# Kernel optimization log

Measured on AMD Instinct MI355X. Metric: run time of the kernel, lower is better.

The kernel has to match this reference:

```python
import jax, jax.numpy as jnp
import numpy as np
import math

DIM = 512
HID = 2048
BS, SLEN = 4, 4096


def _bayes_linear(x, mu, log_sigma, eps):
    # torchbnn BayesLinear: W = mu + exp(log_sigma) * eps; y = x @ W^T
    W = mu + jnp.exp(log_sigma) * eps
    return jnp.einsum('...i,oi->...o', x, W)


def setup_inputs() -> dict:
    key = jax.random.key(0)
    ks = jax.random.split(key, 20)
    d = {}
    d['x'] = jax.random.normal(ks[0], (BS, SLEN, DIM), dtype=jnp.float32)
    # causal additive mask, broadcast over batch
    causal = jnp.triu(jnp.full((SLEN, SLEN), -1e9, dtype=jnp.float32), k=1)
    d['mask'] = causal[None, :, :]
    shapes = {'wk': (DIM, DIM), 'wv': (DIM, DIM), 'wo': (DIM, DIM), 'w1': (HID, DIM), 'w2': (DIM, HID)}
    i = 1
    for name, shp in shapes.items():
        fan_in = shp[1]
        d[name + '_mu'] = jax.random.normal(ks[i], shp, dtype=jnp.float32) / np.sqrt(fan_in); i += 1
        d[name + '_ls'] = (-3.0 + 0.1 * jax.random.normal(ks[i], shp, dtype=jnp.float32)); i += 1
        d[name + '_eps'] = jax.random.normal(ks[i], shp, dtype=jnp.float32); i += 1
    return d


def reference(x, mask, wk_mu, wk_ls, wk_eps, wv_mu, wv_ls, wv_eps, wo_mu, wo_ls, wo_eps,
              w1_mu, w1_ls, w1_eps, w2_mu, w2_ls, w2_eps):
    dim = x.shape[-1]
    # attention: W_q is identity
    xq = x
    xk = _bayes_linear(x, wk_mu, wk_ls, wk_eps)
    xv = _bayes_linear(x, wv_mu, wv_ls, wv_eps)
    scores = jnp.einsum('bqd,bkd->bqk', xq, xk) / math.sqrt(dim) + mask
    attn = jax.nn.softmax(scores, axis=-1)
    h = jnp.einsum('bqk,bkd->bqd', attn, xv)
    h_attn = _bayes_linear(h, wo_mu, wo_ls, wo_eps)
    h_res = x + h_attn
    # FFN with ReLU
    ff = _bayes_linear(h_res, w1_mu, w1_ls, w1_eps)
    ff = jax.nn.relu(ff)
    ff = _bayes_linear(ff, w2_mu, w2_ls, w2_eps)
    return h_res + ff
```

## Files before the change

### kernel.cpp

```cpp
#include <hip/hip_runtime.h>
#include <hip/hip_bf16.h>

typedef __hip_bfloat16 bf16;
typedef __attribute__((ext_vector_type(8))) short short8;
typedef __attribute__((ext_vector_type(4))) float f32x4;

#define MFMA16(a,b,c) __builtin_amdgcn_mfma_f32_16x16x32_bf16(a,b,c,0,0,0)

__device__ __forceinline__ void gl_lds16(const void* g, void* l) {
  __builtin_amdgcn_global_load_lds(
      (const __attribute__((address_space(1))) void*)g,
      (__attribute__((address_space(3))) void*)l, 16, 0, 0);
}

__global__ __launch_bounds__(256) void prep_kernel(
    const float* __restrict__ x,
    const float* __restrict__ m0, const float* __restrict__ l0, const float* __restrict__ e0,
    const float* __restrict__ m1, const float* __restrict__ l1, const float* __restrict__ e1,
    const float* __restrict__ m2, const float* __restrict__ l2, const float* __restrict__ e2,
    const float* __restrict__ m3, const float* __restrict__ l3, const float* __restrict__ e3,
    const float* __restrict__ m4, const float* __restrict__ l4, const float* __restrict__ e4,
    bf16* __restrict__ xb, bf16* __restrict__ wts)
{
  long e = ((long)blockIdx.x * 256 + threadIdx.x) * 4;
  if (e < 8388608L) {
    float4 v = *(const float4*)(x + e);
    union { bf16 b[4]; short4 s; } u;
    u.b[0] = __float2bfloat16(v.x); u.b[1] = __float2bfloat16(v.y);
    u.b[2] = __float2bfloat16(v.z); u.b[3] = __float2bfloat16(v.w);
    *(short4*)(xb + e) = u.s;
  } else {
    long we = e - 8388608L;
    const float *mu, *ls, *ep; long off = we;
    if (we < 262144L)        { mu = m0; ls = l0; ep = e0; }
    else if (we < 524288L)   { mu = m1; ls = l1; ep = e1; off = we - 262144L; }
    else if (we < 786432L)   { mu = m2; ls = l2; ep = e2; off = we - 524288L; }
    else if (we < 1835008L)  { mu = m3; ls = l3; ep = e3; off = we - 786432L; }
    else                     { mu = m4; ls = l4; ep = e4; off = we - 1835008L; }
    float4 a = *(const float4*)(mu + off);
    float4 b = *(const float4*)(ls + off);
    float4 c = *(const float4*)(ep + off);
    union { bf16 w[4]; short4 s; } u;
    u.w[0] = __float2bfloat16(a.x + __expf(b.x) * c.x);
    u.w[1] = __float2bfloat16(a.y + __expf(b.y) * c.y);
    u.w[2] = __float2bfloat16(a.z + __expf(b.z) * c.z);
    u.w[3] = __float2bfloat16(a.w + __expf(b.w) * c.w);
    *(short4*)(wts + we) = u.s;
  }
}

template<int MODE>
__global__ __launch_bounds__(256, 2) void gemm_nt(
    const bf16* __restrict__ A, const bf16* __restrict__ B,
    const float* __restrict__ resid, float* __restrict__ outf,
    bf16* __restrict__ outb, int M, int N, int K)
{
  __shared__ bf16 As[128 * 32];
  __shared__ bf16 Bs[128 * 32];
  const int t = threadIdx.x, w = t >> 6, lane = t & 63;
  const int quad = lane >> 4, c16 = lane & 15;
  const int bm = blockIdx.x << 7, bn = blockIdx.y << 7;
  const int wr = (w >> 1) << 6, wc = (w & 1) << 6;

  f32x4 acc[4][4] = {};

  const int srow = t >> 2;
  const int scol = (t & 3) * 8;
  const bf16* Ab = A + (long)bm * K;
  const bf16* Bb = B + (long)bn * K;

  for (int k0 = 0; k0 < K; k0 += 32) {
    gl_lds16(Ab + (long)srow * K + k0 + scol,        (char*)As + (w << 10));
    gl_lds16(Ab + (long)(64 + srow) * K + k0 + scol, (char*)As + 4096 + (w << 10));
    gl_lds16(Bb + (long)srow * K + k0 + scol,        (char*)Bs + (w << 10));
    gl_lds16(Bb + (long)(64 + srow) * K + k0 + scol, (char*)Bs + 4096 + (w << 10));
    __syncthreads();
    short8 a[4], b[4];
    #pragma unroll
    for (int i = 0; i < 4; i++)
      a[i] = *(const short8*)(As + (wr + i * 16 + c16) * 32 + quad * 8);
    #pragma unroll
    for (int j = 0; j < 4; j++)
      b[j] = *(const short8*)(Bs + (wc + j * 16 + c16) * 32 + quad * 8);
    #pragma unroll
    for (int i = 0; i < 4; i++)
      #pragma unroll
      for (int j = 0; j < 4; j++)
        acc[i][j] = MFMA16(a[i], b[j], acc[i][j]);
    __syncthreads();
  }

  #pragma unroll
  for (int i = 0; i < 4; i++) {
    const int row = bm + wr + i * 16 + quad * 4;
    #pragma unroll
    for (int j = 0; j < 4; j++) {
      const int col = bn + wc + j * 16 + c16;
      #pragma unroll
      for (int r = 0; r < 4; r++) {
        float v = acc[i][j][r];
        if (MODE == 4) {
          int n = (row + r) & 31;
          long idx = (long)(row + r) * 512 + ((((col >> 3) ^ (n & 7)) << 3) | (col & 7));
          outb[idx] = __float2bfloat16(v);
        } else if (MODE == 5) {
          int g = row + r;
          int kvl = g & 31;
          long idx = (((long)(g >> 5)) << 14) + (long)col * 32 +
                     (((kvl >> 3) ^ ((col >> 1) & 3)) << 3) + (kvl & 7);
          outb[idx] = __float2bfloat16(v);
        } else {
          long idx = (long)(row + r) * N + col;
          if (MODE == 0) {
            outb[idx] = __float2bfloat16(v);
          } else if (MODE == 1) {
            float vv = v + resid[idx];
            outf[idx] = vv;
            outb[idx] = __float2bfloat16(vv);
          } else if (MODE == 2) {
            outb[idx] = __float2bfloat16(v > 0.f ? v : 0.f);
          } else {
            outf[idx] = v + resid[idx];
          }
        }
      }
    }
  }
}

__global__ __launch_bounds__(256, 2) void attn3_kernel(
    const bf16* __restrict__ xq, const bf16* __restrict__ xkS,
    const bf16* __restrict__ xvS, bf16* __restrict__ Opart,
    float* __restrict__ lsum)
{
  __shared__ bf16 Ks[32 * 512];
  __shared__ bf16 Vs[512 * 32];
  __shared__ bf16 Pb[4 * 512];

  const int t = threadIdx.x, w = t >> 6, lane = t & 63;
  const int quad = lane >> 4, c16 = lane & 15;
  const int n = blockIdx.x;
  const int B = n & 3, h = (n >> 2) & 1, i = n >> 3;
  const long boff = (long)B * (4096L * 512);
  const float scale = 0.04419417382415922f;
  const float FM = 30.0f;

  union { short8 s; short u[8]; } ones;
  #pragma unroll
  for (int k = 0; k < 8; k++) ones.u[k] = (short)0x3F80;

  for (int seg = 0; seg < 2; seg++) {
    const int qt = seg ? (63 - i) : i;
    const int nt = qt + 1;
    const int t0 = h * nt;
    const int qb = qt << 6;

    short8 qf[16];
    {
      const bf16* qrow = xq + boff + (long)(qb + w * 16 + c16) * 512 + quad * 8;
      #pragma unroll
      for (int f = 0; f < 16; f++) qf[f] = *(const short8*)(qrow + f * 32);
    }

    f32x4 o[32];
    #pragma unroll
    for (int jj = 0; jj < 32; jj++) o[jj] = (f32x4){0.f, 0.f, 0.f, 0.f};
    f32x4 lacc = (f32x4){0.f, 0.f, 0.f, 0.f};

    for (int tt = 0; tt < nt; ++tt) {
      const int tile = t0 + tt;
      const int kv0 = tile << 5;
      {
        const long tb = ((long)(B * 128 + tile)) << 14;
        const bf16* ks = xkS + tb + (w << 9) + (lane << 3);
        const bf16* vs = xvS + tb + (w << 9) + (lane << 3);
        char* kd = (char*)Ks + (w << 10);
        char* vd = (char*)Vs + (w << 10);
        #pragma unroll
        for (int r2 = 0; r2 < 8; r2++) {
          gl_lds16(ks + (r2 << 11), kd + (r2 << 12));
          gl_lds16(vs + (r2 << 11), vd + (r2 << 12));
        }
      }
      __syncthreads();

      f32x4 s0 = (f32x4){0.f, 0.f, 0.f, 0.f};
      f32x4 s1 = s0;
      const int n0 = c16, n1 = 16 + c16;
      const int sw0 = (c16 & 7) << 3;
      #pragma unroll
      for (int f = 0; f < 16; f++) {
        int cb = (f * 4 + quad) << 3;
        short8 b0 = *(const short8*)(Ks + n0 * 512 + (cb ^ sw0));
        short8 b1 = *(const short8*)(Ks + n1 * 512 + (cb ^ sw0));
        s0 = MFMA16(qf[f], b0, s0);
        s1 = MFMA16(qf[f], b1, s1);
      }

      bf16* Pw = Pb + (w << 9);
      {
        const int qr0 = qb + w * 16 + quad * 4;
        const bool need_mask = (kv0 + 32 > qb);
        #pragma unroll
        for (int r = 0; r < 4; r++) {
          float p0 = __expf(fmaf(s0[r], scale, -FM));
          float p1 = __expf(fmaf(s1[r], scale, -FM));
          if (need_mask) {
            if (kv0 + n0 > qr0 + r) p0 = 0.f;
            if (kv0 + n1 > qr0 + r) p1 = 0.f;
          }
          int pr = quad * 4 + r;
          int swp = (pr >> 1) & 3;
          Pw[pr * 32 + (((n0 >> 3) ^ swp) << 3) + (n0 & 7)] = __float2bfloat16(p0);
          Pw[pr * 32 + (((n1 >> 3) ^ swp) << 3) + (n1 & 7)] = __float2bfloat16(p1);
        }
      }
      short8 pa = *(const short8*)(Pw + c16 * 32 + ((quad ^ ((c16 >> 1) & 3)) << 3));
      lacc = MFMA16(pa, ones.s, lacc);
      #pragma unroll
      for (int jj = 0; jj < 32; jj++) {
        int d = jj * 16 + c16;
        short8 vb = *(const short8*)(Vs + d * 32 + ((quad ^ ((d >> 1) & 3)) << 3));
        o[jj] = MFMA16(pa, vb, o[jj]);
      }
      __syncthreads();
    }

    const int pidx = (B * 64 + qt) * 2 + h;
    {
      bf16* ob = Opart + ((long)pidx << 15) + (long)(w * 16 + quad * 4) * 512 + c16;
      #pragma unroll
      for (int r = 0; r < 4; r++) {
        #pragma unroll
        for (int jj = 0; jj < 32; jj++)
          ob[(long)r * 512 + jj * 16] = __float2bfloat16(o[jj][r]);
      }
      if (c16 == 0) {
        #pragma unroll
        for (int r = 0; r < 4; r++)
          lsum[pidx * 64 + w * 16 + quad * 4 + r] = lacc[r];
      }
    }
  }
}

__global__ __launch_bounds__(256) void combine_kernel(
    const bf16* __restrict__ Opart, const float* __restrict__ lsum,
    bf16* __restrict__ hb)
{
  const int t = threadIdx.x;
  const int r = blockIdx.x * 4 + (t >> 6);
  const int B = r >> 12, rl = r & 4095, qt = rl >> 6, rr = rl & 63;
  const int pA = (B * 64 + qt) * 2, pB = pA + 1;
  float inv = 1.0f / (lsum[pA * 64 + rr] + lsum[pB * 64 + rr]);
  const int d0 = (t & 63) * 8;
  union { short8 s; bf16 b[8]; } ua, ub, uo;
  ua.s = *(const short8*)(Opart + (((long)pA << 6) + rr) * 512 + d0);
  ub.s = *(const short8*)(Opart + (((long)pB << 6) + rr) * 512 + d0);
  #pragma unroll
  for (int k = 0; k < 8; k++)
    uo.b[k] = __float2bfloat16((__bfloat162float(ua.b[k]) + __bfloat162float(ub.b[k])) * inv);
  *(short8*)(hb + (long)r * 512 + d0) = uo.s;
}

extern "C" void kernel_launch(void* const* d_in, const int* in_sizes, int n_in,
                              void* d_out, int out_size, void* d_ws, size_t ws_size,
                              hipStream_t stream) {
  (void)in_sizes; (void)n_in; (void)out_size; (void)ws_size;
  const float* x = (const float*)d_in[0];
  const float* wk_mu = (const float*)d_in[2],  *wk_ls = (const float*)d_in[3],  *wk_eps = (const float*)d_in[4];
  const float* wv_mu = (const float*)d_in[5],  *wv_ls = (const float*)d_in[6],  *wv_eps = (const float*)d_in[7];
  const float* wo_mu = (const float*)d_in[8],  *wo_ls = (const float*)d_in[9],  *wo_eps = (const float*)d_in[10];
  const float* w1_mu = (const float*)d_in[11], *w1_ls = (const float*)d_in[12], *w1_eps = (const float*)d_in[13];
  const float* w2_mu = (const float*)d_in[14], *w2_ls = (const float*)d_in[15], *w2_eps = (const float*)d_in[16];

  const long MB = 1048576L;
  char* ws = (char*)d_ws;
  bf16*   xb    = (bf16*)(ws + 0);
  bf16*   xkS   = (bf16*)(ws + 16 * MB);
  bf16*   xvS   = (bf16*)(ws + 32 * MB);
  bf16*   Opart = (bf16*)(ws + 48 * MB);
  float*  lsb   = (float*)(ws + 80 * MB);
  bf16*   wts   = (bf16*)(ws + 113 * MB);
  bf16*   hb    = (bf16*)(ws + 32 * MB);
  bf16*   hrb   = (bf16*)(ws + 64 * MB);
  float*  hrf   = (float*)(ws + 81 * MB);
  bf16*   ffb   = (bf16*)(ws + 0);

  bf16* wkb = wts;
  bf16* wvb = wts + 262144;
  bf16* wob = wts + 524288;
  bf16* w1b = wts + 786432;
  bf16* w2b = wts + 1835008;

  prep_kernel<<<11008, 256, 0, stream>>>(x,
      wk_mu, wk_ls, wk_eps, wv_mu, wv_ls, wv_eps, wo_mu, wo_ls, wo_eps,
      w1_mu, w1_ls, w1_eps, w2_mu, w2_ls, w2_eps, xb, wts);

  gemm_nt<4><<<dim3(128, 4),  256, 0, stream>>>(xb,  wkb, nullptr, nullptr, xkS, 16384, 512, 512);
  gemm_nt<5><<<dim3(128, 4),  256, 0, stream>>>(xb,  wvb, nullptr, nullptr, xvS, 16384, 512, 512);

  attn3_kernel<<<256, 256, 0, stream>>>(xb, xkS, xvS, Opart, lsb);
  combine_kernel<<<4096, 256, 0, stream>>>(Opart, lsb, hb);

  gemm_nt<1><<<dim3(128, 4),  256, 0, stream>>>(hb,  wob, x,   hrf, hrb, 16384, 512, 512);
  gemm_nt<2><<<dim3(128, 16), 256, 0, stream>>>(hrb, w1b, nullptr, nullptr, ffb, 16384, 2048, 512);
  gemm_nt<3><<<dim3(128, 4),  256, 0, stream>>>(ffb, w2b, hrf, (float*)d_out, nullptr, 16384, 512, 2048);
}
```

Measured before the change: 538.8 us.

## Split attention KV range four ways with strided tiles and four-way combine

The attention kernel now splits each query tile's KV range across four blocks (interleaved tiles with stride 4) instead of two contiguous halves, launching 512 blocks instead of 256. The combine kernel sums four partial outputs and four partial row sums. The workspace layout is rearranged to fit the doubled partial buffer. The aim is better CU occupancy and load balance across the 256 CUs. In exchange, the partial outputs written and read back double, and Q fragments are reloaded by more blocks.

```diff
diff --git a/kernel.cpp b/kernel.cpp
--- a/kernel.cpp
+++ b/kernel.cpp
@@ -128,7 +128,7 @@
   }
 }
 
-__global__ __launch_bounds__(256, 2) void attn3_kernel(
+__global__ __launch_bounds__(256, 2) void attn4_kernel(
     const bf16* __restrict__ xq, const bf16* __restrict__ xkS,
     const bf16* __restrict__ xvS, bf16* __restrict__ Opart,
     float* __restrict__ lsum)
@@ -140,7 +140,7 @@
   const int t = threadIdx.x, w = t >> 6, lane = t & 63;
   const int quad = lane >> 4, c16 = lane & 15;
   const int n = blockIdx.x;
-  const int B = n & 3, h = (n >> 2) & 1, i = n >> 3;
+  const int B = n & 3, par = (n >> 2) & 3, i = n >> 4;
   const long boff = (long)B * (4096L * 512);
   const float scale = 0.04419417382415922f;
   const float FM = 30.0f;
@@ -151,8 +151,7 @@
 
   for (int seg = 0; seg < 2; seg++) {
     const int qt = seg ? (63 - i) : i;
-    const int nt = qt + 1;
-    const int t0 = h * nt;
+    const int T = 2 * (qt + 1);
     const int qb = qt << 6;
 
     short8 qf[16];
@@ -167,8 +166,7 @@
     for (int jj = 0; jj < 32; jj++) o[jj] = (f32x4){0.f, 0.f, 0.f, 0.f};
     f32x4 lacc = (f32x4){0.f, 0.f, 0.f, 0.f};
 
-    for (int tt = 0; tt < nt; ++tt) {
-      const int tile = t0 + tt;
+    for (int tile = par; tile < T; tile += 4) {
       const int kv0 = tile << 5;
       {
         const long tb = ((long)(B * 128 + tile)) << 14;
@@ -226,7 +224,7 @@
       __syncthreads();
     }
 
-    const int pidx = (B * 64 + qt) * 2 + h;
+    const int pidx = (B * 64 + qt) * 4 + par;
     {
       bf16* ob = Opart + ((long)pidx << 15) + (long)(w * 16 + quad * 4) * 512 + c16;
       #pragma unroll
@@ -251,15 +249,22 @@
   const int t = threadIdx.x;
   const int r = blockIdx.x * 4 + (t >> 6);
   const int B = r >> 12, rl = r & 4095, qt = rl >> 6, rr = rl & 63;
-  const int pA = (B * 64 + qt) * 2, pB = pA + 1;
-  float inv = 1.0f / (lsum[pA * 64 + rr] + lsum[pB * 64 + rr]);
+  const int p0 = (B * 64 + qt) * 4;
+  float lt = lsum[p0 * 64 + rr] + lsum[(p0 + 1) * 64 + rr] +
+             lsum[(p0 + 2) * 64 + rr] + lsum[(p0 + 3) * 64 + rr];
+  float inv = 1.0f / lt;
   const int d0 = (t & 63) * 8;
-  union { short8 s; bf16 b[8]; } ua, ub, uo;
-  ua.s = *(const short8*)(Opart + (((long)pA << 6) + rr) * 512 + d0);
-  ub.s = *(const short8*)(Opart + (((long)pB << 6) + rr) * 512 + d0);
+  union { short8 s; bf16 b[8]; } u0, u1, u2, u3, uo;
+  u0.s = *(const short8*)(Opart + (((long)(p0 + 0) << 6) + rr) * 512 + d0);
+  u1.s = *(const short8*)(Opart + (((long)(p0 + 1) << 6) + rr) * 512 + d0);
+  u2.s = *(const short8*)(Opart + (((long)(p0 + 2) << 6) + rr) * 512 + d0);
+  u3.s = *(const short8*)(Opart + (((long)(p0 + 3) << 6) + rr) * 512 + d0);
   #pragma unroll
-  for (int k = 0; k < 8; k++)
-    uo.b[k] = __float2bfloat16((__bfloat162float(ua.b[k]) + __bfloat162float(ub.b[k])) * inv);
+  for (int k = 0; k < 8; k++) {
+    float s = __bfloat162float(u0.b[k]) + __bfloat162float(u1.b[k]) +
+              __bfloat162float(u2.b[k]) + __bfloat162float(u3.b[k]);
+    uo.b[k] = __float2bfloat16(s * inv);
+  }
   *(short8*)(hb + (long)r * 512 + d0) = uo.s;
 }
 
@@ -280,11 +285,11 @@
   bf16*   xkS   = (bf16*)(ws + 16 * MB);
   bf16*   xvS   = (bf16*)(ws + 32 * MB);
   bf16*   Opart = (bf16*)(ws + 48 * MB);
-  float*  lsb   = (float*)(ws + 80 * MB);
+  float*  lsb   = (float*)(ws + 112 * MB);
   bf16*   wts   = (bf16*)(ws + 113 * MB);
   bf16*   hb    = (bf16*)(ws + 32 * MB);
-  bf16*   hrb   = (bf16*)(ws + 64 * MB);
-  float*  hrf   = (float*)(ws + 81 * MB);
+  float*  hrf   = (float*)(ws + 64 * MB);
+  bf16*   hrb   = (bf16*)(ws + 96 * MB);
   bf16*   ffb   = (bf16*)(ws + 0);
 
   bf16* wkb = wts;
@@ -300,7 +305,7 @@
   gemm_nt<4><<<dim3(128, 4),  256, 0, stream>>>(xb,  wkb, nullptr, nullptr, xkS, 16384, 512, 512);
   gemm_nt<5><<<dim3(128, 4),  256, 0, stream>>>(xb,  wvb, nullptr, nullptr, xvS, 16384, 512, 512);
 
-  attn3_kernel<<<256, 256, 0, stream>>>(xb, xkS, xvS, Opart, lsb);
+  attn4_kernel<<<512, 256, 0, stream>>>(xb, xkS, xvS, Opart, lsb);
   combine_kernel<<<4096, 256, 0, stream>>>(Opart, lsb, hb);
 
   gemm_nt<1><<<dim3(128, 4),  256, 0, stream>>>(hb,  wob, x,   hrf, hrb, 16384, 512, 512);
```

New measurement: 464.6 us. 13.8% less time.
